# Kernel optimization log

Measured on AMD Instinct MI355X. Metric: run time of the kernel, lower is better.

## Reference

```python
import jax, jax.numpy as jnp
import numpy as np

B, L, D = 2, 2048, 2048
H, G, HD = 16, 4, 128
EPS = 1e-6
THETA_BASE = 10000.0


def setup_inputs() -> dict:
    key = jax.random.key(0)
    ks = jax.random.split(key, 5)
    x = jax.random.normal(ks[0], (B, L, D), jnp.float32)
    Wq = jax.random.normal(ks[1], (D, H * HD), jnp.float32) * 0.02
    Wk = jax.random.normal(ks[2], (D, G * HD), jnp.float32) * 0.02
    Wv = jax.random.normal(ks[3], (D, G * HD), jnp.float32) * 0.02
    Wo = jax.random.normal(ks[4], (H * HD, D), jnp.float32) * 0.02
    q_scale = jnp.ones((HD,), jnp.float32)
    k_scale = jnp.ones((HD,), jnp.float32)
    # Well-formed RoPE tables of shape [L, HD] (duplicated-half layout expected by apply_rope)
    inv_freq = 1.0 / (THETA_BASE ** (jnp.arange(0, HD // 2, dtype=jnp.float32) * 2.0 / HD))  # [HD/2]
    angles = jnp.arange(L, dtype=jnp.float32)[:, None] * inv_freq[None, :]  # [L, HD/2]
    angles = jnp.concatenate([angles, angles], axis=1)  # [L, HD]
    cos = jnp.cos(angles)
    sin = jnp.sin(angles)
    # Causal mask: True = masked (matches masked_fill(mask, -inf))
    mask = jnp.triu(jnp.ones((L, L), dtype=bool), k=1)
    return {"x": x, "Wq": Wq, "Wk": Wk, "Wv": Wv, "Wo": Wo,
            "q_scale": q_scale, "k_scale": k_scale, "cos": cos, "sin": sin, "mask": mask}


def _rmsnorm(x, scale):
    var = jnp.mean(x * x, axis=-1, keepdims=True)
    return x * jax.lax.rsqrt(var + EPS) * scale


def _rope(x, cos, sin):
    # x: [B, h, L, HD]; cos/sin: [L, HD]
    hd = x.shape[-1]
    x1, x2 = x[..., : hd // 2], x[..., hd // 2 :]
    rotated = jnp.concatenate([-x2, x1], axis=-1)
    return x * cos[None, None] + rotated * sin[None, None]


def reference(x, Wq, Wk, Wv, Wo, q_scale, k_scale, cos, sin, mask):
    b, l, _ = x.shape
    q = (x @ Wq).reshape(b, l, H, HD).transpose(0, 2, 1, 3)  # [B,H,L,HD]
    k = (x @ Wk).reshape(b, l, G, HD).transpose(0, 2, 1, 3)  # [B,G,L,HD]
    v = (x @ Wv).reshape(b, l, G, HD).transpose(0, 2, 1, 3)
    q = _rmsnorm(q, q_scale)
    k = _rmsnorm(k, k_scale)
    q = _rope(q, cos, sin)
    k = _rope(k, cos, sin)
    gs = H // G
    k = jnp.repeat(k, gs, axis=1)  # [B,H,L,HD]
    v = jnp.repeat(v, gs, axis=1)
    scores = jnp.einsum('bhqd,bhkd->bhqk', q, k)
    scores = jnp.where(mask, -jnp.inf, scores)
    # NB: faithful to the source's unusual scaling by head_dim**2 (not sqrt)
    w = jax.nn.softmax(scores / float(HD ** 2), axis=-1)
    out = jnp.einsum('bhqk,bhkd->bhqd', w, v).transpose(0, 2, 1, 3).reshape(b, l, H * HD)
    return out @ Wo
```

## Files before the change

### kernel.cpp

```cpp
#include <hip/hip_runtime.h>
#include <math.h>

#define SEQ 2048
#define DMODEL 2048
#define NHQ 16
#define NHK 4

typedef __attribute__((ext_vector_type(8))) short short8;
typedef __attribute__((ext_vector_type(8))) unsigned short ushort8;
typedef __attribute__((ext_vector_type(4))) float floatx4;

#define AS1 __attribute__((address_space(1)))
#define AS3 __attribute__((address_space(3)))

__device__ __forceinline__ unsigned short f2bf(float f) {
  unsigned int u = __builtin_bit_cast(unsigned int, f);
  u += 0x7fffu + ((u >> 16) & 1u);
  return (unsigned short)(u >> 16);
}
__device__ __forceinline__ float bf2f(unsigned short s) {
  unsigned int u = ((unsigned int)s) << 16;
  return __builtin_bit_cast(float, u);
}

__global__ __launch_bounds__(256) void prep(const float* __restrict__ x,
                                            const float* __restrict__ Wq,
                                            const float* __restrict__ Wk,
                                            const float* __restrict__ Wv,
                                            const float* __restrict__ Wo,
                                            unsigned short* __restrict__ x_bf,
                                            unsigned short* __restrict__ wqkv_t,
                                            unsigned short* __restrict__ wo_t) {
  const int z = blockIdx.z;
  const int tx = threadIdx.x, ty = threadIdx.y;
  const int tid = ty * 32 + tx;
  if (z == 3) {
    const size_t base = ((size_t)(blockIdx.y * 64 + blockIdx.x)) * 4096 + (size_t)tid * 16;
    const float4 v0 = *(const float4*)(x + base);
    const float4 v1 = *(const float4*)(x + base + 4);
    const float4 v2 = *(const float4*)(x + base + 8);
    const float4 v3 = *(const float4*)(x + base + 12);
    ushort8 w0, w1;
    w0[0] = f2bf(v0.x); w0[1] = f2bf(v0.y); w0[2] = f2bf(v0.z); w0[3] = f2bf(v0.w);
    w0[4] = f2bf(v1.x); w0[5] = f2bf(v1.y); w0[6] = f2bf(v1.z); w0[7] = f2bf(v1.w);
    w1[0] = f2bf(v2.x); w1[1] = f2bf(v2.y); w1[2] = f2bf(v2.z); w1[3] = f2bf(v2.w);
    w1[4] = f2bf(v3.x); w1[5] = f2bf(v3.y); w1[6] = f2bf(v3.z); w1[7] = f2bf(v3.w);
    *(ushort8*)(x_bf + base) = w0;
    *(ushort8*)(x_bf + base + 8) = w1;
    return;
  }
  int bx = blockIdx.x;
  const float* in;
  unsigned short* out;
  int C;
  const int R = 2048;
  if (z == 0)      { in = Wq; out = wqkv_t;                          C = 2048; }
  else if (z == 1) { in = Wo; out = wo_t;                            C = 2048; }
  else {
    if (bx < 16)      { in = Wk; out = wqkv_t + (size_t)2048 * 2048; C = 512; }
    else if (bx < 32) { in = Wv; out = wqkv_t + (size_t)2560 * 2048; C = 512; bx -= 16; }
    else return;
  }
  __shared__ float tile[32][65];
  const int c0 = bx * 32, r0 = blockIdx.y * 64;
#pragma unroll
  for (int j = 0; j < 8; ++j)
    tile[tx][ty + j * 8] = in[(size_t)(r0 + ty + j * 8) * C + c0 + tx];
  __syncthreads();
  const int c = tid >> 3;
  const int l8 = tid & 7;
  ushort8 w;
#pragma unroll
  for (int u = 0; u < 8; ++u) w[u] = f2bf(tile[c][l8 * 8 + u]);
  *(ushort8*)(out + (size_t)(c0 + c) * R + r0 + l8 * 8) = w;
}

#define PBAR() do { __builtin_amdgcn_sched_barrier(0); __builtin_amdgcn_s_barrier(); \
                    __builtin_amdgcn_sched_barrier(0); } while (0)
#define KWAIT8(deep) do { if (deep) asm volatile("s_waitcnt vmcnt(8)" ::: "memory"); \
                          else      asm volatile("s_waitcnt vmcnt(0)" ::: "memory"); } while (0)
#define KWAIT6(deep) do { if (deep) asm volatile("s_waitcnt vmcnt(6)" ::: "memory"); \
                          else      asm volatile("s_waitcnt vmcnt(0)" ::: "memory"); } while (0)

__device__ __forceinline__ void mfma_q(floatx4 (&ac)[4][4],
                                       const short8 (&a)[4], const short8 (&b)[4]) {
#pragma unroll
  for (int i = 0; i < 4; ++i)
#pragma unroll
    for (int j = 0; j < 4; ++j)
      ac[i][j] = __builtin_amdgcn_mfma_f32_16x16x32_bf16(a[i], b[j], ac[i][j], 0, 0, 0);
}

__device__ __forceinline__ void ld4(short8 (&v)[4], const unsigned short* p) {
#pragma unroll
  for (int i = 0; i < 4; ++i) v[i] = *(const short8*)(p + i * 512);
}

__device__ __forceinline__ void stg_half(const unsigned short* src0,
                                         unsigned short* dst_uniform) {
  __builtin_amdgcn_global_load_lds((const AS1 void*)src0,
                                   (AS3 void*)dst_uniform, 16, 0, 0);
  __builtin_amdgcn_global_load_lds((const AS1 void*)(src0 + (size_t)128 * 2048),
                                   (AS3 void*)(dst_uniform + 4096), 16, 0, 0);
}
__device__ __forceinline__ void stg_halfA(const unsigned short* src0,
                                          unsigned short* dst_uniform) {
  __builtin_amdgcn_global_load_lds((const AS1 void*)src0,
                                   (AS3 void*)dst_uniform, 16, 0, 0);
}

__device__ __forceinline__ void kloop256(const unsigned short* __restrict__ A,
                                         const unsigned short* __restrict__ Bt,
                                         unsigned short* ldsA, unsigned short* ldsB,
                                         int bm, int bn, int tid,
                                         floatx4 (&accL)[4][4], floatx4 (&accH)[4][4]) {
  const int wave = tid >> 6;
  const int lane = tid & 63;
  const int m15 = lane & 15;
  const int quad = lane >> 4;
  const int wr = wave >> 2;
  const int wcol = wave & 3;

  const int srow = tid >> 2;
  const int csrc = ((tid & 3) ^ ((tid >> 3) & 3)) * 8;
  const unsigned short* gA = A + (size_t)(bm + srow) * 2048 + csrc;
  const unsigned short* gB = Bt + (size_t)(bn + srow) * 2048 + csrc;
  const int wslot = wave * 512;

  const int rc = (quad ^ ((m15 >> 1) & 3)) * 8;
  const int aoff = (wr * 128 + m15) * 32 + rc;
  const int boff = (wcol * 64 + m15) * 32 + rc;

  stg_half(gA + 0,  ldsA + wslot);
  stg_half(gB + 0,  ldsB + wslot);
  stg_half(gA + 32, ldsA + 8192 + wslot);
  stg_half(gB + 32, ldsB + 8192 + wslot);
  stg_half(gA + 64, ldsA + 16384 + wslot);
  stg_half(gB + 64, ldsB + 16384 + wslot);
  asm volatile("s_waitcnt vmcnt(0)" ::: "memory");
  __builtin_amdgcn_s_barrier();
  __builtin_amdgcn_sched_barrier(0);

  const int NK = 32;
  short8 af[4], bv[4];
  for (int t = 0; t < NK; ++t) {
    const int d = t & 1;
    unsigned short* Ab0 = ldsA + d * 16384;
    unsigned short* Bb0 = ldsB + d * 16384;
    unsigned short* Aalt = ldsA + (d ^ 1) * 16384;
    unsigned short* Balt = ldsB + (d ^ 1) * 16384;
    const bool st1 = (t + 1 < NK), st2 = (t + 2 < NK);
    const int k1 = (t + 1) * 64 + 32;
    const int k2 = (t + 2) * 64;

    ld4(af, Ab0 + aoff);
    ld4(bv, Bb0 + boff);
    if (st1) stg_half(gA + k1, Aalt + 8192 + wslot);
    PBAR();
    __builtin_amdgcn_s_setprio(1);
    mfma_q(accL, af, bv);
    __builtin_amdgcn_s_setprio(0);
    PBAR();

    ld4(af, Ab0 + aoff + 2048);
    if (st1) stg_half(gB + k1, Balt + 8192 + wslot);
    PBAR();
    __builtin_amdgcn_s_setprio(1);
    mfma_q(accH, af, bv);
    __builtin_amdgcn_s_setprio(0);
    KWAIT8(st2);
    PBAR();

    ld4(af, Ab0 + 8192 + aoff);
    ld4(bv, Bb0 + 8192 + boff);
    if (st2) stg_half(gA + k2, Ab0 + wslot);
    PBAR();
    __builtin_amdgcn_s_setprio(1);
    mfma_q(accL, af, bv);
    __builtin_amdgcn_s_setprio(0);
    PBAR();

    ld4(af, Ab0 + 8192 + aoff + 2048);
    if (st2) stg_half(gB + k2, Bb0 + wslot);
    PBAR();
    __builtin_amdgcn_s_setprio(1);
    mfma_q(accH, af, bv);
    __builtin_amdgcn_s_setprio(0);
    KWAIT8(st2);
    PBAR();
  }
}

__global__ __launch_bounds__(512, 2) void gemm_qkv_fused(const unsigned short* __restrict__ A,
                                                         const unsigned short* __restrict__ Bt,
                                                         unsigned short* __restrict__ qout,
                                                         unsigned short* __restrict__ kout,
                                                         unsigned short* __restrict__ vout,
                                                         const float* __restrict__ q_scale,
                                                         const float* __restrict__ k_scale,
                                                         const float* __restrict__ cosb,
                                                         const float* __restrict__ sinb) {
  __shared__ unsigned short lds[65536];
  unsigned short* ldsA = lds;
  unsigned short* ldsB = lds + 32768;

  const int tid = threadIdx.x;
  const int wave = tid >> 6;
  const int lane = tid & 63;
  const int m15 = lane & 15;
  const int quad = lane >> 4;
  const int wr = wave >> 2;
  const int wcol = wave & 3;
  const int bxn = blockIdx.x;
  const int bm = blockIdx.y * 256;
  const int bn = bxn * 256;

  floatx4 accL[4][4], accH[4][4];
#pragma unroll
  for (int i = 0; i < 4; ++i)
#pragma unroll
    for (int j = 0; j < 4; ++j) {
      accL[i][j] = (floatx4){0.f, 0.f, 0.f, 0.f};
      accH[i][j] = (floatx4){0.f, 0.f, 0.f, 0.f};
    }

  kloop256(A, Bt, ldsA, ldsB, bm, bn, tid, accL, accH);

  unsigned short* epi = lds;
  const int b = bm >> 11;
  const int l_base = bm & (SEQ - 1);
  const int t64 = tid & 63;

  for (int c = 0; c < 2; ++c) {
    __syncthreads();
    if ((wcol >> 1) == c) {
      const int colb = (wcol & 1) * 64;
#pragma unroll
      for (int i = 0; i < 4; ++i)
#pragma unroll
        for (int j = 0; j < 4; ++j)
#pragma unroll
          for (int r = 0; r < 4; ++r) {
            epi[(wr * 128 + i * 16 + quad * 4 + r) * 129 + colb + j * 16 + m15] =
                f2bf(accL[i][j][r]);
            epi[(wr * 128 + 64 + i * 16 + quad * 4 + r) * 129 + colb + j * 16 + m15] =
                f2bf(accH[i][j][r]);
          }
    }
    __syncthreads();

    const int hh = 2 * bxn + c;
    if (hh < 20) {
      const float* scale = (hh < NHQ) ? q_scale : k_scale;
      unsigned short* dstbase = (hh < NHQ)
          ? qout + ((size_t)(b * NHQ + hh) * SEQ + l_base) * 128
          : kout + ((size_t)(b * NHK + (hh - NHQ)) * SEQ + l_base) * 128;
      const float sc0 = scale[t64];
      const float sc1 = scale[t64 + 64];
#pragma unroll 4
      for (int rr = 0; rr < 32; ++rr) {
        const int row = wave * 32 + rr;
        const float v0 = bf2f(epi[row * 129 + t64]);
        const float v1 = bf2f(epi[row * 129 + t64 + 64]);
        float ss = v0 * v0 + v1 * v1;
#pragma unroll
        for (int m = 1; m < 64; m <<= 1) ss += __shfl_xor(ss, m);
        const float r = rsqrtf(ss * (1.0f / 128.0f) + 1e-6f);
        const int l = l_base + row;
        const float c0v = cosb[(size_t)l * 128 + t64];
        const float s0 = sinb[(size_t)l * 128 + t64];
        const float c1v = cosb[(size_t)l * 128 + t64 + 64];
        const float s1 = sinb[(size_t)l * 128 + t64 + 64];
        const float a0 = v0 * r * sc0;
        const float a1 = v1 * r * sc1;
        unsigned short* dst = dstbase + (size_t)row * 128;
        dst[t64]      = f2bf(a0 * c0v - a1 * s0);
        dst[t64 + 64] = f2bf(a1 * c1v + a0 * s1);
      }
    } else {
      const int g = hh - 20;
      unsigned short* vbase = vout + (size_t)(b * NHK + g) * 128 * SEQ + l_base;
#pragma unroll 4
      for (int dd = 0; dd < 16; ++dd) {
        const int d = wave * 16 + dd;
        unsigned short* dst = vbase + (size_t)d * SEQ;
        dst[t64]       = epi[t64 * 129 + d];
        dst[t64 + 64]  = epi[(t64 + 64) * 129 + d];
        dst[t64 + 128] = epi[(t64 + 128) * 129 + d];
        dst[t64 + 192] = epi[(t64 + 192) * 129 + d];
      }
    }
  }
}

__global__ __launch_bounds__(512, 2) void gemm_bf16_f32(const unsigned short* __restrict__ A,
                                                        const unsigned short* __restrict__ Bt,
                                                        float* __restrict__ C,
                                                        int M, int N, int K) {
  __shared__ unsigned short lds[49152];
  unsigned short* ldsA = lds;
  unsigned short* ldsB = lds + 16384;

  const int tid = threadIdx.x;
  const int wave = tid >> 6;
  const int lane = tid & 63;
  const int m15 = lane & 15;
  const int quad = lane >> 4;
  const int wr = wave >> 2;
  const int wcol = wave & 3;
  const int bm = blockIdx.y * 128;
  const int bn = blockIdx.x * 256;

  floatx4 acc[4][4];
#pragma unroll
  for (int i = 0; i < 4; ++i)
#pragma unroll
    for (int j = 0; j < 4; ++j) acc[i][j] = (floatx4){0.f, 0.f, 0.f, 0.f};

  const int srow = tid >> 2;
  const int csrc = ((tid & 3) ^ ((tid >> 3) & 3)) * 8;
  const unsigned short* gA = A + (size_t)(bm + srow) * 2048 + csrc;
  const unsigned short* gB = Bt + (size_t)(bn + srow) * 2048 + csrc;
  const int wslot = wave * 512;

  const int rc = (quad ^ ((m15 >> 1) & 3)) * 8;
  const int aoff = (wr * 64 + m15) * 32 + rc;
  const int boff = (wcol * 64 + m15) * 32 + rc;

  stg_halfA(gA + 0,  ldsA + wslot);
  stg_half (gB + 0,  ldsB + wslot);
  stg_halfA(gA + 32, ldsA + 4096 + wslot);
  stg_half (gB + 32, ldsB + 8192 + wslot);
  stg_halfA(gA + 64, ldsA + 8192 + wslot);
  stg_half (gB + 64, ldsB + 16384 + wslot);
  asm volatile("s_waitcnt vmcnt(0)" ::: "memory");
  __builtin_amdgcn_s_barrier();
  __builtin_amdgcn_sched_barrier(0);

  const int NK = 32;
  short8 af[4], bv[4];
  for (int t = 0; t < NK; ++t) {
    const int d = t & 1;
    unsigned short* Ab = ldsA + d * 8192;
    unsigned short* Bb = ldsB + d * 16384;
    unsigned short* Aalt = ldsA + (d ^ 1) * 8192;
    unsigned short* Balt = ldsB + (d ^ 1) * 16384;
    const bool st1 = (t + 1 < NK), st2 = (t + 2 < NK);
    const int k1 = (t + 1) * 64 + 32;
    const int k2 = (t + 2) * 64;

    ld4(af, Ab + aoff);
    ld4(bv, Bb + boff);
    if (st1) { stg_halfA(gA + k1, Aalt + 4096 + wslot);
               stg_half (gB + k1, Balt + 8192 + wslot); }
    PBAR();
    __builtin_amdgcn_s_setprio(1);
    mfma_q(acc, af, bv);
    __builtin_amdgcn_s_setprio(0);
    KWAIT6(st2);
    PBAR();

    ld4(af, Ab + 4096 + aoff);
    ld4(bv, Bb + 8192 + boff);
    if (st2) { stg_halfA(gA + k2, Ab + wslot);
               stg_half (gB + k2, Bb + wslot); }
    PBAR();
    __builtin_amdgcn_s_setprio(1);
    mfma_q(acc, af, bv);
    __builtin_amdgcn_s_setprio(0);
    KWAIT6(st2);
    PBAR();
  }

#pragma unroll
  for (int i = 0; i < 4; ++i)
#pragma unroll
    for (int j = 0; j < 4; ++j)
#pragma unroll
      for (int r = 0; r < 4; ++r) {
        const int col = bn + wcol * 64 + j * 16 + m15;
        C[(size_t)(bm + wr * 64 + i * 16 + quad * 4 + r) * N + col] = acc[i][j][r];
      }
}

__global__ __launch_bounds__(256, 4) void attn_mfma(const unsigned short* __restrict__ qb,
                                                    const unsigned short* __restrict__ kb,
                                                    const unsigned short* __restrict__ vtb,
                                                    unsigned short* __restrict__ o) {
  __shared__ unsigned short Ks[64 * 128];
  __shared__ unsigned short Vs[128 * 64];
  unsigned short* Ps = Ks;

  const int tid = threadIdx.x;
  const int wave = tid >> 6;
  const int lane = tid & 63;
  const int m15 = lane & 15;
  const int quad = lane >> 4;
  const int bh = blockIdx.x;
  const int b = bh >> 4;
  const int h = bh & 15;
  const int g = h >> 2;
  const int q0 = ((int)gridDim.y - 1 - (int)blockIdx.y) * 64;

  const unsigned short* qhead = qb + (size_t)bh * SEQ * 128;
  const unsigned short* khead = kb + (size_t)(b * NHK + g) * SEQ * 128;
  const unsigned short* vthead = vtb + (size_t)(b * NHK + g) * 128 * SEQ;

  short8 qf[4];
  {
    const unsigned short* qp = qhead + (size_t)(q0 + wave * 16 + m15) * 128 + quad * 8;
#pragma unroll
    for (int ks = 0; ks < 4; ++ks) qf[ks] = *(const short8*)(qp + ks * 32);
  }

  floatx4 acc_o[8];
#pragma unroll
  for (int n = 0; n < 8; ++n) acc_o[n] = (floatx4){0.f, 0.f, 0.f, 0.f};
  float l_lane[4] = {0.f, 0.f, 0.f, 0.f};
  const float inv_scale = 1.0f / 16384.0f;

  for (int j0 = 0; j0 <= q0; j0 += 64) {
#pragma unroll
    for (int t = 0; t < 4; ++t) {
      const int r = wave * 16 + t * 4 + (lane >> 4);
      const int cg = (lane & 15) ^ (r & 15);
      const unsigned short* src = khead + (size_t)(j0 + r) * 128 + cg * 8;
      __builtin_amdgcn_global_load_lds(
          (const AS1 void*)src,
          (AS3 void*)&Ks[(wave * 16 + t * 4) * 128], 16, 0, 0);
    }
#pragma unroll
    for (int t = 0; t < 4; ++t) {
      const int d = wave * 32 + t * 8 + (lane >> 3);
      const int cg = (lane & 7) ^ (d & 7);
      const unsigned short* src = vthead + (size_t)d * SEQ + j0 + cg * 8;
      __builtin_amdgcn_global_load_lds(
          (const AS1 void*)src,
          (AS3 void*)&Vs[(wave * 32 + t * 8) * 64], 16, 0, 0);
    }
    __syncthreads();

    floatx4 acc_s[4];
#pragma unroll
    for (int n = 0; n < 4; ++n) acc_s[n] = (floatx4){0.f, 0.f, 0.f, 0.f};
#pragma unroll
    for (int ks = 0; ks < 4; ++ks) {
#pragma unroll
      for (int n = 0; n < 4; ++n) {
        const short8 bfrag = *(const short8*)&Ks[(n * 16 + m15) * 128 + (((ks * 4 + quad) ^ m15) * 8)];
        acc_s[n] = __builtin_amdgcn_mfma_f32_16x16x32_bf16(qf[ks], bfrag, acc_s[n], 0, 0, 0);
      }
    }
    __syncthreads();

    if (j0 == q0) {
      const int row_g = wave * 16 + quad * 4;
#pragma unroll
      for (int n = 0; n < 4; ++n) {
        const int col = n * 16 + m15;
#pragma unroll
        for (int rg = 0; rg < 4; ++rg) {
          float p = (col > row_g + rg) ? 0.0f : __expf(acc_s[n][rg] * inv_scale);
          l_lane[rg] += p;
          Ps[(wave * 16 + quad * 4 + rg) * 72 + n * 16 + m15] = f2bf(p);
        }
      }
    } else {
#pragma unroll
      for (int n = 0; n < 4; ++n) {
#pragma unroll
        for (int rg = 0; rg < 4; ++rg) {
          const float p = __expf(acc_s[n][rg] * inv_scale);
          l_lane[rg] += p;
          Ps[(wave * 16 + quad * 4 + rg) * 72 + n * 16 + m15] = f2bf(p);
        }
      }
    }

#pragma unroll
    for (int kk = 0; kk < 2; ++kk) {
      const short8 a = *(const short8*)&Ps[(wave * 16 + m15) * 72 + kk * 32 + quad * 8];
#pragma unroll
      for (int n = 0; n < 8; ++n) {
        const short8 bfrag = *(const short8*)&Vs[(n * 16 + m15) * 64 + (((kk * 4 + quad) ^ (m15 & 7)) * 8)];
        acc_o[n] = __builtin_amdgcn_mfma_f32_16x16x32_bf16(a, bfrag, acc_o[n], 0, 0, 0);
      }
    }
    __syncthreads();
  }

#pragma unroll
  for (int rg = 0; rg < 4; ++rg) {
    float l = l_lane[rg];
    l += __shfl_xor(l, 1);
    l += __shfl_xor(l, 2);
    l += __shfl_xor(l, 4);
    l += __shfl_xor(l, 8);
    const float invl = 1.0f / l;
    const size_t row = (size_t)(b * SEQ + q0 + wave * 16 + quad * 4 + rg);
#pragma unroll
    for (int n = 0; n < 8; ++n)
      o[row * DMODEL + h * 128 + n * 16 + m15] = f2bf(acc_o[n][rg] * invl);
  }
}

extern "C" void kernel_launch(void* const* d_in, const int* in_sizes, int n_in,
                              void* d_out, int out_size, void* d_ws, size_t ws_size,
                              hipStream_t stream) {
  const float* x       = (const float*)d_in[0];
  const float* Wq      = (const float*)d_in[1];
  const float* Wk      = (const float*)d_in[2];
  const float* Wv      = (const float*)d_in[3];
  const float* Wo      = (const float*)d_in[4];
  const float* q_scale = (const float*)d_in[5];
  const float* k_scale = (const float*)d_in[6];
  const float* cosb    = (const float*)d_in[7];
  const float* sinb    = (const float*)d_in[8];
  float* out = (float*)d_out;

  char* w = (char*)d_ws;
  unsigned short* x_bf    = (unsigned short*)w;
  unsigned short* wqkv_t  = (unsigned short*)(w + 16777216);
  unsigned short* q_bf    = (unsigned short*)(w + 29360128);
  unsigned short* k_bf    = (unsigned short*)(w + 46137344);
  unsigned short* vt      = (unsigned short*)(w + 50331648);
  unsigned short* wo_t    = (unsigned short*)(w + 54525952);
  unsigned short* attn_bf = (unsigned short*)(w + 62914560);

  prep<<<dim3(64, 32, 4), dim3(32, 8), 0, stream>>>(x, Wq, Wk, Wv, Wo, x_bf, wqkv_t, wo_t);

  gemm_qkv_fused<<<dim3(12, 16), 512, 0, stream>>>(x_bf, wqkv_t, q_bf, k_bf, vt,
                                                   q_scale, k_scale, cosb, sinb);

  attn_mfma<<<dim3(2 * NHQ, SEQ / 64), 256, 0, stream>>>(q_bf, k_bf, vt, attn_bf);

  gemm_bf16_f32<<<dim3(2048 / 256, 4096 / 128), 512, 0, stream>>>(
      attn_bf, wo_t, out, 4096, 2048, 2048);
}
```

Measured before the change: 304.4 us.

## Retile fused QKV GEMM to 128x384 blocks for full CU occupancy

Changes the QKV projection GEMM tile from 256x256 to 128x384, launching 8x32=256 blocks instead of 192. Each block covers three heads, and the epilogue is reworked for three head chunks with 128 rows. The aim is to fill all CUs in a single wave rather than leaving some idle. In exchange, the B tile is reread across more row blocks and the per-wave register footprint for the 4x6 accumulators grows.

Result: no change. 301.0 us (-1.1%).

```diff
diff --git a/kernel.cpp b/kernel.cpp
--- a/kernel.cpp
+++ b/kernel.cpp
@@ -95,100 +95,31 @@
 #pragma unroll
   for (int i = 0; i < 4; ++i) v[i] = *(const short8*)(p + i * 512);
 }
-
-__device__ __forceinline__ void stg_half(const unsigned short* src0,
-                                         unsigned short* dst_uniform) {
+__device__ __forceinline__ void ld6(short8 (&v)[6], const unsigned short* p) {
+#pragma unroll
+  for (int i = 0; i < 6; ++i) v[i] = *(const short8*)(p + i * 512);
+}
+
+__device__ __forceinline__ void stg1(const unsigned short* src0,
+                                     unsigned short* dst_uniform) {
+  __builtin_amdgcn_global_load_lds((const AS1 void*)src0,
+                                   (AS3 void*)dst_uniform, 16, 0, 0);
+}
+__device__ __forceinline__ void stg2(const unsigned short* src0,
+                                     unsigned short* dst_uniform) {
   __builtin_amdgcn_global_load_lds((const AS1 void*)src0,
                                    (AS3 void*)dst_uniform, 16, 0, 0);
   __builtin_amdgcn_global_load_lds((const AS1 void*)(src0 + (size_t)128 * 2048),
                                    (AS3 void*)(dst_uniform + 4096), 16, 0, 0);
 }
-__device__ __forceinline__ void stg_halfA(const unsigned short* src0,
-                                          unsigned short* dst_uniform) {
+__device__ __forceinline__ void stg3(const unsigned short* src0,
+                                     unsigned short* dst_uniform) {
   __builtin_amdgcn_global_load_lds((const AS1 void*)src0,
                                    (AS3 void*)dst_uniform, 16, 0, 0);
-}
-
-__device__ __forceinline__ void kloop256(const unsigned short* __restrict__ A,
-                                         const unsigned short* __restrict__ Bt,
-                                         unsigned short* ldsA, unsigned short* ldsB,
-                                         int bm, int bn, int tid,
-                                         floatx4 (&accL)[4][4], floatx4 (&accH)[4][4]) {
-  const int wave = tid >> 6;
-  const int lane = tid & 63;
-  const int m15 = lane & 15;
-  const int quad = lane >> 4;
-  const int wr = wave >> 2;
-  const int wcol = wave & 3;
-
-  const int srow = tid >> 2;
-  const int csrc = ((tid & 3) ^ ((tid >> 3) & 3)) * 8;
-  const unsigned short* gA = A + (size_t)(bm + srow) * 2048 + csrc;
-  const unsigned short* gB = Bt + (size_t)(bn + srow) * 2048 + csrc;
-  const int wslot = wave * 512;
-
-  const int rc = (quad ^ ((m15 >> 1) & 3)) * 8;
-  const int aoff = (wr * 128 + m15) * 32 + rc;
-  const int boff = (wcol * 64 + m15) * 32 + rc;
-
-  stg_half(gA + 0,  ldsA + wslot);
-  stg_half(gB + 0,  ldsB + wslot);
-  stg_half(gA + 32, ldsA + 8192 + wslot);
-  stg_half(gB + 32, ldsB + 8192 + wslot);
-  stg_half(gA + 64, ldsA + 16384 + wslot);
-  stg_half(gB + 64, ldsB + 16384 + wslot);
-  asm volatile("s_waitcnt vmcnt(0)" ::: "memory");
-  __builtin_amdgcn_s_barrier();
-  __builtin_amdgcn_sched_barrier(0);
-
-  const int NK = 32;
-  short8 af[4], bv[4];
-  for (int t = 0; t < NK; ++t) {
-    const int d = t & 1;
-    unsigned short* Ab0 = ldsA + d * 16384;
-    unsigned short* Bb0 = ldsB + d * 16384;
-    unsigned short* Aalt = ldsA + (d ^ 1) * 16384;
-    unsigned short* Balt = ldsB + (d ^ 1) * 16384;
-    const bool st1 = (t + 1 < NK), st2 = (t + 2 < NK);
-    const int k1 = (t + 1) * 64 + 32;
-    const int k2 = (t + 2) * 64;
-
-    ld4(af, Ab0 + aoff);
-    ld4(bv, Bb0 + boff);
-    if (st1) stg_half(gA + k1, Aalt + 8192 + wslot);
-    PBAR();
-    __builtin_amdgcn_s_setprio(1);
-    mfma_q(accL, af, bv);
-    __builtin_amdgcn_s_setprio(0);
-    PBAR();
-
-    ld4(af, Ab0 + aoff + 2048);
-    if (st1) stg_half(gB + k1, Balt + 8192 + wslot);
-    PBAR();
-    __builtin_amdgcn_s_setprio(1);
-    mfma_q(accH, af, bv);
-    __builtin_amdgcn_s_setprio(0);
-    KWAIT8(st2);
-    PBAR();
-
-    ld4(af, Ab0 + 8192 + aoff);
-    ld4(bv, Bb0 + 8192 + boff);
-    if (st2) stg_half(gA + k2, Ab0 + wslot);
-    PBAR();
-    __builtin_amdgcn_s_setprio(1);
-    mfma_q(accL, af, bv);
-    __builtin_amdgcn_s_setprio(0);
-    PBAR();
-
-    ld4(af, Ab0 + 8192 + aoff + 2048);
-    if (st2) stg_half(gB + k2, Bb0 + wslot);
-    PBAR();
-    __builtin_amdgcn_s_setprio(1);
-    mfma_q(accH, af, bv);
-    __builtin_amdgcn_s_setprio(0);
-    KWAIT8(st2);
-    PBAR();
-  }
+  __builtin_amdgcn_global_load_lds((const AS1 void*)(src0 + (size_t)128 * 2048),
+                                   (AS3 void*)(dst_uniform + 4096), 16, 0, 0);
+  __builtin_amdgcn_global_load_lds((const AS1 void*)(src0 + (size_t)256 * 2048),
+                                   (AS3 void*)(dst_uniform + 8192), 16, 0, 0);
 }
 
 __global__ __launch_bounds__(512, 2) void gemm_qkv_fused(const unsigned short* __restrict__ A,
@@ -202,7 +133,7 @@
                                                          const float* __restrict__ sinb) {
   __shared__ unsigned short lds[65536];
   unsigned short* ldsA = lds;
-  unsigned short* ldsB = lds + 32768;
+  unsigned short* ldsB = lds + 16384;
 
   const int tid = threadIdx.x;
   const int wave = tid >> 6;
@@ -212,44 +143,100 @@
   const int wr = wave >> 2;
   const int wcol = wave & 3;
   const int bxn = blockIdx.x;
-  const int bm = blockIdx.y * 256;
-  const int bn = bxn * 256;
-
-  floatx4 accL[4][4], accH[4][4];
+  const int bm = blockIdx.y * 128;
+  const int bn = bxn * 384;
+
+  floatx4 acc[4][6];
 #pragma unroll
   for (int i = 0; i < 4; ++i)
 #pragma unroll
-    for (int j = 0; j < 4; ++j) {
-      accL[i][j] = (floatx4){0.f, 0.f, 0.f, 0.f};
-      accH[i][j] = (floatx4){0.f, 0.f, 0.f, 0.f};
-    }
-
-  kloop256(A, Bt, ldsA, ldsB, bm, bn, tid, accL, accH);
+    for (int j = 0; j < 6; ++j) acc[i][j] = (floatx4){0.f, 0.f, 0.f, 0.f};
+
+  const int srow = tid >> 2;
+  const int csrc = ((tid & 3) ^ ((tid >> 3) & 3)) * 8;
+  const unsigned short* gA = A + (size_t)(bm + srow) * 2048 + csrc;
+  const unsigned short* gB = Bt + (size_t)(bn + srow) * 2048 + csrc;
+  const int wslot = wave * 512;
+
+  const int rc = (quad ^ ((m15 >> 1) & 3)) * 8;
+  const int aoff = (wr * 64 + m15) * 32 + rc;
+  const int boff = (wcol * 96 + m15) * 32 + rc;
+
+  stg1(gA + 0,  ldsA + wslot);
+  stg3(gB + 0,  ldsB + wslot);
+  stg1(gA + 32, ldsA + 4096 + wslot);
+  stg3(gB + 32, ldsB + 12288 + wslot);
+  stg1(gA + 64, ldsA + 8192 + wslot);
+  stg3(gB + 64, ldsB + 24576 + wslot);
+  asm volatile("s_waitcnt vmcnt(0)" ::: "memory");
+  __builtin_amdgcn_s_barrier();
+  __builtin_amdgcn_sched_barrier(0);
+
+  const int NK = 32;
+  short8 af[4], bv[6];
+  for (int t = 0; t < NK; ++t) {
+    const int d = t & 1;
+    unsigned short* Ab = ldsA + d * 8192;
+    unsigned short* Bb = ldsB + d * 24576;
+    unsigned short* Aalt = ldsA + (d ^ 1) * 8192;
+    unsigned short* Balt = ldsB + (d ^ 1) * 24576;
+    const bool st1 = (t + 1 < NK), st2 = (t + 2 < NK);
+    const int k1 = (t + 1) * 64 + 32;
+    const int k2 = (t + 2) * 64;
+
+    ld4(af, Ab + aoff);
+    ld6(bv, Bb + boff);
+    if (st1) { stg1(gA + k1, Aalt + 4096 + wslot);
+               stg3(gB + k1, Balt + 12288 + wslot); }
+    PBAR();
+    __builtin_amdgcn_s_setprio(1);
+#pragma unroll
+    for (int i = 0; i < 4; ++i)
+#pragma unroll
+      for (int j = 0; j < 6; ++j)
+        acc[i][j] = __builtin_amdgcn_mfma_f32_16x16x32_bf16(af[i], bv[j], acc[i][j], 0, 0, 0);
+    __builtin_amdgcn_s_setprio(0);
+    KWAIT8(st2);
+    PBAR();
+
+    ld4(af, Ab + 4096 + aoff);
+    ld6(bv, Bb + 12288 + boff);
+    if (st2) { stg1(gA + k2, Ab + wslot);
+               stg3(gB + k2, Bb + wslot); }
+    PBAR();
+    __builtin_amdgcn_s_setprio(1);
+#pragma unroll
+    for (int i = 0; i < 4; ++i)
+#pragma unroll
+      for (int j = 0; j < 6; ++j)
+        acc[i][j] = __builtin_amdgcn_mfma_f32_16x16x32_bf16(af[i], bv[j], acc[i][j], 0, 0, 0);
+    __builtin_amdgcn_s_setprio(0);
+    KWAIT8(st2);
+    PBAR();
+  }
 
   unsigned short* epi = lds;
   const int b = bm >> 11;
   const int l_base = bm & (SEQ - 1);
   const int t64 = tid & 63;
 
-  for (int c = 0; c < 2; ++c) {
+  for (int c = 0; c < 3; ++c) {
     __syncthreads();
-    if ((wcol >> 1) == c) {
-      const int colb = (wcol & 1) * 64;
-#pragma unroll
-      for (int i = 0; i < 4; ++i)
-#pragma unroll
-        for (int j = 0; j < 4; ++j)
-#pragma unroll
-          for (int r = 0; r < 4; ++r) {
-            epi[(wr * 128 + i * 16 + quad * 4 + r) * 129 + colb + j * 16 + m15] =
-                f2bf(accL[i][j][r]);
-            epi[(wr * 128 + 64 + i * 16 + quad * 4 + r) * 129 + colb + j * 16 + m15] =
-                f2bf(accH[i][j][r]);
-          }
+#pragma unroll
+    for (int j = 0; j < 6; ++j) {
+      const int head16 = 6 * wcol + j;
+      if ((head16 >> 3) == c) {
+        const int incol = (head16 & 7) * 16 + m15;
+#pragma unroll
+        for (int i = 0; i < 4; ++i)
+#pragma unroll
+          for (int r = 0; r < 4; ++r)
+            epi[(wr * 64 + i * 16 + quad * 4 + r) * 129 + incol] = f2bf(acc[i][j][r]);
+      }
     }
     __syncthreads();
 
-    const int hh = 2 * bxn + c;
+    const int hh = 3 * bxn + c;
     if (hh < 20) {
       const float* scale = (hh < NHQ) ? q_scale : k_scale;
       unsigned short* dstbase = (hh < NHQ)
@@ -258,8 +245,8 @@
       const float sc0 = scale[t64];
       const float sc1 = scale[t64 + 64];
 #pragma unroll 4
-      for (int rr = 0; rr < 32; ++rr) {
-        const int row = wave * 32 + rr;
+      for (int rr = 0; rr < 16; ++rr) {
+        const int row = wave * 16 + rr;
         const float v0 = bf2f(epi[row * 129 + t64]);
         const float v1 = bf2f(epi[row * 129 + t64 + 64]);
         float ss = v0 * v0 + v1 * v1;
@@ -282,12 +269,10 @@
       unsigned short* vbase = vout + (size_t)(b * NHK + g) * 128 * SEQ + l_base;
 #pragma unroll 4
       for (int dd = 0; dd < 16; ++dd) {
-        const int d = wave * 16 + dd;
-        unsigned short* dst = vbase + (size_t)d * SEQ;
-        dst[t64]       = epi[t64 * 129 + d];
-        dst[t64 + 64]  = epi[(t64 + 64) * 129 + d];
-        dst[t64 + 128] = epi[(t64 + 128) * 129 + d];
-        dst[t64 + 192] = epi[(t64 + 192) * 129 + d];
+        const int dcol = wave * 16 + dd;
+        unsigned short* dst = vbase + (size_t)dcol * SEQ;
+        dst[t64]      = epi[t64 * 129 + dcol];
+        dst[t64 + 64] = epi[(t64 + 64) * 129 + dcol];
       }
     }
   }
@@ -327,12 +312,12 @@
   const int aoff = (wr * 64 + m15) * 32 + rc;
   const int boff = (wcol * 64 + m15) * 32 + rc;
 
-  stg_halfA(gA + 0,  ldsA + wslot);
-  stg_half (gB + 0,  ldsB + wslot);
-  stg_halfA(gA + 32, ldsA + 4096 + wslot);
-  stg_half (gB + 32, ldsB + 8192 + wslot);
-  stg_halfA(gA + 64, ldsA + 8192 + wslot);
-  stg_half (gB + 64, ldsB + 16384 + wslot);
+  stg1(gA + 0,  ldsA + wslot);
+  stg2(gB + 0,  ldsB + wslot);
+  stg1(gA + 32, ldsA + 4096 + wslot);
+  stg2(gB + 32, ldsB + 8192 + wslot);
+  stg1(gA + 64, ldsA + 8192 + wslot);
+  stg2(gB + 64, ldsB + 16384 + wslot);
   asm volatile("s_waitcnt vmcnt(0)" ::: "memory");
   __builtin_amdgcn_s_barrier();
   __builtin_amdgcn_sched_barrier(0);
@@ -351,8 +336,8 @@
 
     ld4(af, Ab + aoff);
     ld4(bv, Bb + boff);
-    if (st1) { stg_halfA(gA + k1, Aalt + 4096 + wslot);
-               stg_half (gB + k1, Balt + 8192 + wslot); }
+    if (st1) { stg1(gA + k1, Aalt + 4096 + wslot);
+               stg2(gB + k1, Balt + 8192 + wslot); }
     PBAR();
     __builtin_amdgcn_s_setprio(1);
     mfma_q(acc, af, bv);
@@ -362,8 +347,8 @@
 
     ld4(af, Ab + 4096 + aoff);
     ld4(bv, Bb + 8192 + boff);
-    if (st2) { stg_halfA(gA + k2, Ab + wslot);
-               stg_half (gB + k2, Bb + wslot); }
+    if (st2) { stg1(gA + k2, Ab + wslot);
+               stg2(gB + k2, Bb + wslot); }
     PBAR();
     __builtin_amdgcn_s_setprio(1);
     mfma_q(acc, af, bv);
@@ -529,8 +514,8 @@
 
   prep<<<dim3(64, 32, 4), dim3(32, 8), 0, stream>>>(x, Wq, Wk, Wv, Wo, x_bf, wqkv_t, wo_t);
 
-  gemm_qkv_fused<<<dim3(12, 16), 512, 0, stream>>>(x_bf, wqkv_t, q_bf, k_bf, vt,
-                                                   q_scale, k_scale, cosb, sinb);
+  gemm_qkv_fused<<<dim3(8, 32), 512, 0, stream>>>(x_bf, wqkv_t, q_bf, k_bf, vt,
+                                                  q_scale, k_scale, cosb, sinb);
 
   attn_mfma<<<dim3(2 * NHQ, SEQ / 64), 256, 0, stream>>>(q_bf, k_bf, vt, attn_bf);
 
```
